# Performance work log

Measured on AMD Instinct MI355X. Metric: run time of the kernel, lower is better.

## Reference

```python
import jax, jax.numpy as jnp
import numpy as np
import math

N, E, R = 50000, 800000, 32
DIN = 128
H, D = 8, 16          # num_heads, head_dim; H*D == out_ent_feats == 128
HOP = 5
ALPHA = 0.1
EPS = 1e-5


def layer_norm(x, g, b):
    m = jnp.mean(x, axis=-1, keepdims=True)
    v = jnp.mean((x - m) ** 2, axis=-1, keepdims=True)
    return (x - m) * jax.lax.rsqrt(v + EPS) * g + b


def segment_softmax(e, dst, num_nodes):
    # e: [E, H] scores, softmax over incoming edges of each dst node
    m = jax.ops.segment_max(e, dst, num_segments=num_nodes)      # [N, H]
    ex = jnp.exp(e - m[dst])
    s = jax.ops.segment_sum(ex, dst, num_segments=num_nodes)     # [N, H]
    return ex / s[dst]


def setup_inputs() -> dict:
    key = jax.random.key(0)
    ks = jax.random.split(key, 12)
    gain = 0.02  # small init scale (small_init_gain-style)
    ent_feat = jax.random.normal(ks[0], (N, DIN), dtype=jnp.float32)
    rel_feat = jax.random.normal(ks[1], (R, DIN), dtype=jnp.float32)
    src = jax.random.randint(ks[2], (E,), 0, N, dtype=jnp.int32)
    # guarantee every node has in-degree >= 1 (DGL raises otherwise)
    dst_rand = jax.random.randint(ks[3], (E - N,), 0, N, dtype=jnp.int32)
    dst = jnp.concatenate([jnp.arange(N, dtype=jnp.int32), dst_rand])
    rid = jax.random.randint(ks[4], (E,), 0, R, dtype=jnp.int32)
    W_head = jax.random.normal(ks[5], (DIN, H * D), dtype=jnp.float32) * gain
    W_tail = jax.random.normal(ks[6], (DIN, H * D), dtype=jnp.float32) * gain
    W_ent = jax.random.normal(ks[7], (DIN, H * D), dtype=jnp.float32) * gain
    W_rel = jax.random.normal(ks[8], (DIN, H * D), dtype=jnp.float32) * gain
    attn_r = jax.random.normal(ks[9], (1, H, D), dtype=jnp.float32) * gain
    W1 = jax.random.normal(ks[10], (H * D, 4 * H * D), dtype=jnp.float32) * gain
    W2 = jax.random.normal(ks[11], (4 * H * D, H * D), dtype=jnp.float32) * gain
    return dict(
        ent_feat=ent_feat, rel_feat=rel_feat, src=src, dst=dst, rid=rid,
        W_head=W_head, W_tail=W_tail, W_ent=W_ent, W_rel=W_rel, attn_r=attn_r,
        ln_ent_g=jnp.ones((DIN,), jnp.float32), ln_ent_b=jnp.zeros((DIN,), jnp.float32),
        ln_rel_g=jnp.ones((DIN,), jnp.float32), ln_rel_b=jnp.zeros((DIN,), jnp.float32),
        ff_ln_g=jnp.ones((H * D,), jnp.float32), ff_ln_b=jnp.zeros((H * D,), jnp.float32),
        W1=W1, b1=jnp.zeros((4 * H * D,), jnp.float32),
        W2=W2, b2=jnp.zeros((H * D,), jnp.float32),
    )


def _forward(ent_feat, rel_feat, src, dst, rid,
             W_head, W_tail, W_ent, W_rel, attn_r,
             ln_ent_g, ln_ent_b, ln_rel_g, ln_rel_b, ff_ln_g, ff_ln_b,
             W1, b1, W2, b2):
    n = ent_feat.shape[0]
    x = layer_norm(ent_feat, ln_ent_g, ln_ent_b)
    feat_head = (x @ W_head).reshape(n, H, D)
    feat_tail = (x @ W_tail).reshape(n, H, D)
    feat_ent = (x @ W_ent).reshape(n, H, D)

    # per-edge dot-product attention score: u_dot_v('eh','et')
    e = jnp.sum(feat_head[src] * feat_tail[dst], axis=-1)          # [E, H]

    r = layer_norm(rel_feat, ln_rel_g, ln_rel_b)
    feat_rel = (r @ W_rel).reshape(R, H, D)
    er = jnp.sum(feat_rel * attn_r, axis=-1)                       # [R, H]
    e = e * er[rid]                                                # [E, H]

    # e_mul_v with log_in = log(in_degree) of dst node
    deg = jax.ops.segment_sum(jnp.ones((e.shape[0],), e.dtype), dst, num_segments=n)
    log_in = jnp.log(jnp.maximum(deg, 1.0))                        # [N]
    e = e * log_in[dst][:, None] / math.sqrt(D)

    a = segment_softmax(e, dst, n)                                 # [E, H]

    # PPR diffusion: feat <- (1-alpha) * A^T feat + alpha * feat_0
    feat = feat_ent
    for _ in range(HOP):
        msg = feat[src] * a[:, :, None]                            # [E, H, D]
        agg = jax.ops.segment_sum(msg, dst, num_segments=n)        # [N, H, D]
        feat = (1.0 - ALPHA) * agg + ALPHA * feat_ent

    # residual (Identity: in_ent_feats == out_ent_feats)
    rst = feat + ent_feat.reshape(n, H, D)
    rst = rst.reshape(n, H * D)

    h = layer_norm(rst, ff_ln_g, ff_ln_b)
    ff = jax.nn.relu(h @ W1 + b1) @ W2 + b2
    return ff + rst


def reference(ent_feat, rel_feat, src, dst, rid,
              W_head, W_tail, W_ent, W_rel, attn_r,
              ln_ent_g, ln_ent_b, ln_rel_g, ln_rel_b, ff_ln_g, ff_ln_b,
              W1, b1, W2, b2):
    return _forward(ent_feat, rel_feat, src, dst, rid,
                    W_head, W_tail, W_ent, W_rel, attn_r,
                    ln_ent_g, ln_ent_b, ln_rel_g, ln_rel_b, ff_ln_g, ff_ln_b,
                    W1, b1, W2, b2)
```

## Files before the change

kernel.cpp:

```cpp
#include <hip/hip_runtime.h>
#include <hip/hip_bf16.h>

#define N_NODES 50000
#define N_EDGES 800000
#define N_REL 32
#define DIN 128
#define NH 8
#define HD 16
#define FF_HID 512
#define EPS_LN 1e-5f

typedef __attribute__((ext_vector_type(8))) short bf16x8;
typedef __attribute__((ext_vector_type(4))) float f32x4;
typedef __attribute__((ext_vector_type(2))) float f32x2;
typedef unsigned short ushort_t;
typedef unsigned int uint_t;

static __device__ __forceinline__ unsigned short f2bf(float f) {
    union { float f; unsigned u; } v; v.f = f;
    unsigned r = (v.u + 0x7fffu + ((v.u >> 16) & 1u)) >> 16;
    return (unsigned short)r;
}
static __device__ __forceinline__ float bf2f(unsigned u16) {
    union { unsigned u; float f; } v; v.u = u16 << 16; return v.f;
}
static __device__ __forceinline__ unsigned char f2fp8(float f) {
    return (unsigned char)(__builtin_amdgcn_cvt_pk_fp8_f32(f, f, 0, false) & 0xff);
}
static __device__ __forceinline__ ushort_t f2fp8x2(float x0, float x1) {
    return (ushort_t)(__builtin_amdgcn_cvt_pk_fp8_f32(x0, x1, 0, false) & 0xffff);
}

static __device__ __forceinline__ void pack_dev(const float* __restrict__ W,
                                                short* __restrict__ out, int K, int Ncols,
                                                int idx) {
    int KT = K >> 5;
    int l = idx & 63;
    int tile = idx >> 6;
    int kt = tile & (KT - 1);
    int ct = tile / KT;
    int c = ct * 16 + (l & 15);
    int k0 = kt * 32 + ((l >> 4) * 8);
    bf16x8 v;
#pragma unroll
    for (int j = 0; j < 8; j++) v[j] = (short)f2bf(W[(size_t)(k0 + j) * Ncols + c]);
    *(bf16x8*)(out + (size_t)idx * 8) = v;
}

#define C0_HIST 512
__global__ __launch_bounds__(256) void combo0_kernel(
    const int* __restrict__ dst, int* __restrict__ deg, const float* __restrict__ W1,
    short* __restrict__ W1p, const float* __restrict__ W2, short* __restrict__ W2p,
    const float* __restrict__ Wh, short* __restrict__ Whp, const float* __restrict__ Wt,
    short* __restrict__ Wtp, const float* __restrict__ We, short* __restrict__ Wep,
    const float* __restrict__ rel_feat, const float* __restrict__ gr,
    const float* __restrict__ br, const float* __restrict__ W_rel,
    const float* __restrict__ attn_r, float* __restrict__ er) {
    __shared__ float red[128];
    __shared__ float xsr[128];
    __shared__ float prod[128];
    int b = blockIdx.x, tid = threadIdx.x;
    if (b < C0_HIST) {
        int i = b * 256 + tid;
        int stride = C0_HIST * 256;
        for (; i < N_EDGES; i += stride) atomicAdd(&deg[dst[i]], 1);
    } else if (b < C0_HIST + 32) {
        pack_dev(W1, W1p, DIN, FF_HID, (b - C0_HIST) * 256 + tid);
    } else if (b < C0_HIST + 64) {
        pack_dev(W2, W2p, FF_HID, DIN, (b - C0_HIST - 32) * 256 + tid);
    } else if (b < C0_HIST + 72) {
        pack_dev(Wh, Whp, DIN, DIN, (b - C0_HIST - 64) * 256 + tid);
    } else if (b < C0_HIST + 80) {
        pack_dev(Wt, Wtp, DIN, DIN, (b - C0_HIST - 72) * 256 + tid);
    } else if (b < C0_HIST + 88) {
        pack_dev(We, Wep, DIN, DIN, (b - C0_HIST - 80) * 256 + tid);
    } else {
        int r = b - (C0_HIST + 88);
        float x = 0.f;
        if (tid < 128) {
            x = rel_feat[r * DIN + tid];
            red[tid] = x;
        }
        __syncthreads();
        for (int off = 64; off > 0; off >>= 1) {
            if (tid < off) red[tid] += red[tid + off];
            __syncthreads();
        }
        float mean = red[0] * (1.f / DIN);
        __syncthreads();
        if (tid < 128) red[tid] = x * x;
        __syncthreads();
        for (int off = 64; off > 0; off >>= 1) {
            if (tid < off) red[tid] += red[tid + off];
            __syncthreads();
        }
        float var = red[0] * (1.f / DIN) - mean * mean;
        float rs = rsqrtf(var + EPS_LN);
        if (tid < 128) xsr[tid] = (x - mean) * rs * gr[tid] + br[tid];
        __syncthreads();
        if (tid < 128) {
            float acc = 0.f;
            for (int k = 0; k < DIN; k++) acc += xsr[k] * W_rel[k * DIN + tid];
            prod[tid] = acc * attn_r[tid];
        }
        __syncthreads();
        if (tid < NH) {
            float s = 0.f;
            for (int d = 0; d < HD; d++) s += prod[tid * HD + d];
            er[r * NH + tid] = s;
        }
    }
}

__global__ __launch_bounds__(1024) void scan2_kernel(const int* __restrict__ deg,
                                                     int* __restrict__ row_off, int n) {
    __shared__ int lds[1024];
    __shared__ int wsum[16];
    __shared__ int s_base;
    int b = blockIdx.x, tid = threadIdx.x;
    int start = b * 1024;
    int partial = 0;
    for (int i = tid; i < start; i += 1024) partial += deg[i];
    for (int m = 32; m > 0; m >>= 1) partial += __shfl_down(partial, m);
    int wid = tid >> 6, lane = tid & 63;
    if (lane == 0) wsum[wid] = partial;
    __syncthreads();
    if (tid == 0) {
        int s = 0;
#pragma unroll
        for (int w = 0; w < 16; w++) s += wsum[w];
        s_base = s;
    }
    int i = start + tid;
    int v = (i < n) ? deg[i] : 0;
    lds[tid] = v;
    __syncthreads();
    for (int off = 1; off < 1024; off <<= 1) {
        int t = (tid >= off) ? lds[tid - off] : 0;
        __syncthreads();
        lds[tid] += t;
        __syncthreads();
    }
    int base = s_base;
    if (i < n) row_off[i] = base + lds[tid] - v;
    if (i == n - 1) row_off[n] = base + lds[tid];
}

#define C1_SCAT 8192
#define NRANGE_DIV 6250
__global__ __launch_bounds__(256) void combo1_kernel(
    const int* __restrict__ src, const int* __restrict__ dst, const int* __restrict__ rid,
    const int* __restrict__ row_off, int* __restrict__ cursor, int* __restrict__ sr_perm,
    const float* __restrict__ ent, const float* __restrict__ g, const float* __restrict__ b,
    const short* __restrict__ Whp, const short* __restrict__ Wtp,
    const short* __restrict__ Wep, unsigned char* __restrict__ head_fp8,
    ushort_t* __restrict__ tail_bf, ushort_t* __restrict__ entp_bf,
    unsigned char* __restrict__ entp_fp8) {
    __shared__ float xs[32][128];
    __shared__ short hsb[32][136];
    int blk = blockIdx.x, tid = threadIdx.x;
    if (blk < C1_SCAT) {
        const int chunk = (N_EDGES + 1023) / 1024;
        int range = blk & 7;
        int slice = blk >> 3;
        int lo = range * NRANGE_DIV, hi = lo + NRANGE_DIV;
        int i0 = slice * chunk;
        int i1 = min(i0 + chunk, N_EDGES);
        for (int i = i0 + tid; i < i1; i += 256) {
            int u = dst[i];
            if (u >= lo && u < hi) {
                int p = row_off[u] + atomicAdd(&cursor[u], 1);
                sr_perm[p] = src[i] | (rid[i] << 16);
            }
        }
        return;
    }
    int base = (blk - C1_SCAT) * 32;
    {
        int c = tid & 127, rb = tid >> 7;
#pragma unroll
        for (int j = 0; j < 16; j++) {
            int r = j * 2 + rb;
            int row = base + r;
            xs[r][c] = (row < N_NODES) ? ent[(size_t)row * DIN + c] : 0.f;
        }
    }
    __syncthreads();
    int wave = tid >> 6, lane = tid & 63;
    {
        float g0 = g[lane], g1 = g[lane + 64], bb0 = b[lane], bb1 = b[lane + 64];
        for (int r = wave * 8; r < wave * 8 + 8; r++) {
            float x0 = xs[r][lane], x1 = xs[r][lane + 64];
            float s1 = x0 + x1, s2 = x0 * x0 + x1 * x1;
            for (int m = 1; m < 64; m <<= 1) {
                s1 += __shfl_xor(s1, m);
                s2 += __shfl_xor(s2, m);
            }
            float mean = s1 * (1.f / DIN);
            float var = s2 * (1.f / DIN) - mean * mean;
            float rs = rsqrtf(var + EPS_LN);
            hsb[r][lane] = (short)f2bf((x0 - mean) * rs * g0 + bb0);
            hsb[r][lane + 64] = (short)f2bf((x1 - mean) * rs * g1 + bb1);
        }
    }
    __syncthreads();
    bf16x8 a[2][4];
#pragma unroll
    for (int rt = 0; rt < 2; rt++)
#pragma unroll
        for (int kt = 0; kt < 4; kt++)
            a[rt][kt] = *(const bf16x8*)&hsb[rt * 16 + (lane & 15)][kt * 32 + (lane >> 4) * 8];
#pragma unroll
    for (int m = 0; m < 3; m++) {
        const bf16x8* bp = (m == 0)   ? (const bf16x8*)Whp
                           : (m == 1) ? (const bf16x8*)Wtp
                                      : (const bf16x8*)Wep;
#pragma unroll
        for (int c2 = 0; c2 < 2; c2++) {
            int ct = wave * 2 + c2;
            f32x4 acc0 = {0.f, 0.f, 0.f, 0.f}, acc1 = {0.f, 0.f, 0.f, 0.f};
#pragma unroll
            for (int kt = 0; kt < 4; kt++) {
                bf16x8 bf = bp[(ct * 4 + kt) * 64 + lane];
                acc0 = __builtin_amdgcn_mfma_f32_16x16x32_bf16(a[0][kt], bf, acc0, 0, 0, 0);
                acc1 = __builtin_amdgcn_mfma_f32_16x16x32_bf16(a[1][kt], bf, acc1, 0, 0, 0);
            }
            int col = ct * 16 + (lane & 15);
            int r0 = (lane >> 4) * 4;
#pragma unroll
            for (int j = 0; j < 4; j++) {
                int row0 = base + r0 + j, row1 = base + 16 + r0 + j;
                if (m == 0) {
                    if (row0 < N_NODES) head_fp8[(size_t)row0 * DIN + col] = f2fp8(acc0[j]);
                    if (row1 < N_NODES) head_fp8[(size_t)row1 * DIN + col] = f2fp8(acc1[j]);
                } else if (m == 1) {
                    if (row0 < N_NODES) tail_bf[(size_t)row0 * DIN + col] = f2bf(acc0[j]);
                    if (row1 < N_NODES) tail_bf[(size_t)row1 * DIN + col] = f2bf(acc1[j]);
                } else {
                    if (row0 < N_NODES) {
                        entp_bf[(size_t)row0 * DIN + col] = f2bf(acc0[j]);
                        entp_fp8[(size_t)row0 * DIN + col] = f2fp8(acc0[j]);
                    }
                    if (row1 < N_NODES) {
                        entp_bf[(size_t)row1 * DIN + col] = f2bf(acc1[j]);
                        entp_fp8[(size_t)row1 * DIN + col] = f2fp8(acc1[j]);
                    }
                }
            }
        }
    }
}

__global__ __launch_bounds__(256) void scores_kernel(
    const unsigned char* __restrict__ head_fp8, const ushort_t* __restrict__ tail_bf,
    const float* __restrict__ er, const int* __restrict__ row_off,
    const int* __restrict__ sr_perm, ushort_t* __restrict__ a_bf,
    float* __restrict__ inv9) {
    int wid = threadIdx.x >> 6;
    int u = blockIdx.x * 4 + wid;
    int lane = threadIdx.x & 63;
    int h = lane & 7, esub = lane >> 3;
    int p0 = row_off[u], p1 = row_off[u + 1];
    int deg = p1 - p0;
    float scale = logf((float)(deg > 0 ? deg : 1)) * 0.25f;
    float t[16];
    {
        const uint_t* tp = (const uint_t*)(tail_bf + (size_t)u * DIN + h * HD);
#pragma unroll
        for (int i = 0; i < 8; i++) {
            uint_t w = tp[i];
            t[2 * i] = bf2f(w & 0xffffu);
            t[2 * i + 1] = bf2f(w >> 16);
        }
    }
    float ssum = 0.f;
    for (int p = p0 + esub; p < p1; p += 8) {
        int v = sr_perm[p];
        int s = v & 0xffff;
        int rr = v >> 16;
        const uint_t* hp = (const uint_t*)(head_fp8 + (size_t)s * DIN + h * HD);
        float dot = 0.f;
#pragma unroll
        for (int i = 0; i < 4; i++) {
            uint_t w = hp[i];
            f32x2 lo = __builtin_amdgcn_cvt_pk_f32_fp8(w, false);
            f32x2 hi = __builtin_amdgcn_cvt_pk_f32_fp8(w, true);
            dot += lo.x * t[4 * i] + lo.y * t[4 * i + 1] + hi.x * t[4 * i + 2] +
                   hi.y * t[4 * i + 3];
        }
        float e = dot * er[rr * NH + h] * scale;
        float sx = expf(e);
        a_bf[(size_t)p * NH + h] = f2bf(sx);
        ssum += sx;
    }
    ssum += __shfl_xor(ssum, 8);
    ssum += __shfl_xor(ssum, 16);
    ssum += __shfl_xor(ssum, 32);
    if (lane < 8) inv9[(size_t)u * NH + lane] = 0.9f / ssum;
}

template <bool OUT_BF>
__global__ __launch_bounds__(256) void diffuse8_kernel(
    const unsigned char* __restrict__ fin8, const ushort_t* __restrict__ entp_bf,
    const ushort_t* __restrict__ a_bf, const int* __restrict__ sr_perm,
    const int* __restrict__ row_off, const float* __restrict__ inv9,
    void* __restrict__ fout) {
    int wid = threadIdx.x >> 6;
    int u = blockIdx.x * 4 + wid;
    int lane = threadIdx.x & 63;
    int hh = lane >> 3;
    int p0 = row_off[u], p1 = row_off[u + 1];
    float acc0 = 0.f, acc1 = 0.f;
    int p = p0;
    for (; p + 8 <= p1; p += 8) {
        int sv[8];
        float av[8];
        ushort_t wv[8];
#pragma unroll
        for (int k = 0; k < 8; k++) sv[k] = sr_perm[p + k] & 0xffff;
#pragma unroll
        for (int k = 0; k < 8; k++) av[k] = bf2f(a_bf[(size_t)(p + k) * NH + hh]);
#pragma unroll
        for (int k = 0; k < 8; k++)
            wv[k] = *(const ushort_t*)(fin8 + (size_t)sv[k] * DIN + 2 * lane);
#pragma unroll
        for (int k = 0; k < 8; k++) {
            f32x2 v = __builtin_amdgcn_cvt_pk_f32_fp8(wv[k], false);
            acc0 += av[k] * v.x;
            acc1 += av[k] * v.y;
        }
    }
    for (; p < p1; ++p) {
        int s0 = sr_perm[p] & 0xffff;
        float a0 = bf2f(a_bf[(size_t)p * NH + hh]);
        uint_t w0 = *(const ushort_t*)(fin8 + (size_t)s0 * DIN + 2 * lane);
        f32x2 v0 = __builtin_amdgcn_cvt_pk_f32_fp8(w0, false);
        acc0 += a0 * v0.x;
        acc1 += a0 * v0.y;
    }
    float iv = inv9[(size_t)u * NH + hh];
    size_t o = (size_t)u * DIN + 2 * lane;
    uint_t e = *(const uint_t*)(entp_bf + o);
    float x0 = iv * acc0 + 0.1f * bf2f(e & 0xffffu);
    float x1 = iv * acc1 + 0.1f * bf2f(e >> 16);
    if (OUT_BF) {
        *(uint_t*)((ushort_t*)fout + o) = (uint_t)f2bf(x0) | ((uint_t)f2bf(x1) << 16);
    } else {
        *(ushort_t*)((unsigned char*)fout + o) = f2fp8x2(x0, x1);
    }
}

static __device__ __forceinline__ int hid_idx(int row, int col) {
    return row * 512 + ((((col >> 3) & 63) ^ (row & 7)) << 3) + (col & 7);
}
__global__ __launch_bounds__(256) void ffn_mfma_kernel(
    const ushort_t* __restrict__ feat, const float* __restrict__ ent0,
    const float* __restrict__ g, const float* __restrict__ b,
    const short* __restrict__ W1p, const float* __restrict__ b1,
    const short* __restrict__ W2p, const float* __restrict__ b2,
    float* __restrict__ out) {
    __shared__ ushort_t rst_bf[16][136];
    __shared__ short hs[16][136];
    __shared__ short hid[16 * 512];
    int tid = threadIdx.x;
    int base = blockIdx.x * 16;
    int wave = tid >> 6, lane = tid & 63;
    {
        int c = tid & 127, rb = tid >> 7;
#pragma unroll
        for (int j = 0; j < 8; j++) {
            int r = j * 2 + rb;
            int row = base + r;
            float v = 0.f;
            if (row < N_NODES) {
                size_t idx = (size_t)row * DIN + c;
                v = bf2f(feat[idx]) + ent0[idx];
            }
            rst_bf[r][c] = f2bf(v);
        }
    }
    __syncthreads();
    {
        float g0 = g[lane], g1 = g[lane + 64], bb0 = b[lane], bb1 = b[lane + 64];
        for (int r = wave * 4; r < wave * 4 + 4; r++) {
            float x0 = bf2f(rst_bf[r][lane]), x1 = bf2f(rst_bf[r][lane + 64]);
            float s1 = x0 + x1, s2 = x0 * x0 + x1 * x1;
            for (int m = 1; m < 64; m <<= 1) {
                s1 += __shfl_xor(s1, m);
                s2 += __shfl_xor(s2, m);
            }
            float mean = s1 * (1.f / DIN);
            float var = s2 * (1.f / DIN) - mean * mean;
            float rs = rsqrtf(var + EPS_LN);
            hs[r][lane] = (short)f2bf((x0 - mean) * rs * g0 + bb0);
            hs[r][lane + 64] = (short)f2bf((x1 - mean) * rs * g1 + bb1);
        }
    }
    __syncthreads();
    {
        bf16x8 a[4];
#pragma unroll
        for (int kt = 0; kt < 4; kt++)
            a[kt] = *(const bf16x8*)&hs[lane & 15][kt * 32 + (lane >> 4) * 8];
        const bf16x8* bp = (const bf16x8*)W1p;
        for (int cti = 0; cti < 8; cti++) {
            int ct = wave * 8 + cti;
            f32x4 acc0 = {0.f, 0.f, 0.f, 0.f};
#pragma unroll
            for (int kt = 0; kt < 4; kt++) {
                bf16x8 bf = bp[(ct * 4 + kt) * 64 + lane];
                acc0 = __builtin_amdgcn_mfma_f32_16x16x32_bf16(a[kt], bf, acc0, 0, 0, 0);
            }
            int col = ct * 16 + (lane & 15);
            float bv = b1[col];
            int r0 = (lane >> 4) * 4;
#pragma unroll
            for (int j = 0; j < 4; j++)
                hid[hid_idx(r0 + j, col)] = (short)f2bf(fmaxf(acc0[j] + bv, 0.f));
        }
    }
    __syncthreads();
    {
        f32x4 acc[2] = {{0.f, 0.f, 0.f, 0.f}, {0.f, 0.f, 0.f, 0.f}};
        const bf16x8* bp2 = (const bf16x8*)W2p;
        for (int kt = 0; kt < 16; kt++) {
            int col8 = kt * 32 + (lane >> 4) * 8;
            bf16x8 a0 = *(const bf16x8*)&hid[hid_idx(lane & 15, col8)];
#pragma unroll
            for (int c2 = 0; c2 < 2; c2++) {
                int ct = wave * 2 + c2;
                bf16x8 bf = bp2[(ct * 16 + kt) * 64 + lane];
                acc[c2] = __builtin_amdgcn_mfma_f32_16x16x32_bf16(a0, bf, acc[c2], 0, 0, 0);
            }
        }
#pragma unroll
        for (int c2 = 0; c2 < 2; c2++) {
            int col = (wave * 2 + c2) * 16 + (lane & 15);
            float bv = b2[col];
            int r0 = (lane >> 4) * 4;
#pragma unroll
            for (int j = 0; j < 4; j++) {
                int row = base + r0 + j;
                if (row < N_NODES)
                    out[(size_t)row * DIN + col] = acc[c2][j] + bv + bf2f(rst_bf[r0 + j][col]);
            }
        }
    }
}

extern "C" void kernel_launch(void* const* d_in, const int* in_sizes, int n_in,
                              void* d_out, int out_size, void* d_ws, size_t ws_size,
                              hipStream_t stream) {
    const float* ent_feat = (const float*)d_in[0];
    const float* rel_feat = (const float*)d_in[1];
    const int* src = (const int*)d_in[2];
    const int* dst = (const int*)d_in[3];
    const int* rid = (const int*)d_in[4];
    const float* W_head = (const float*)d_in[5];
    const float* W_tail = (const float*)d_in[6];
    const float* W_ent = (const float*)d_in[7];
    const float* W_rel = (const float*)d_in[8];
    const float* attn_r = (const float*)d_in[9];
    const float* ln_ent_g = (const float*)d_in[10];
    const float* ln_ent_b = (const float*)d_in[11];
    const float* ln_rel_g = (const float*)d_in[12];
    const float* ln_rel_b = (const float*)d_in[13];
    const float* ff_ln_g = (const float*)d_in[14];
    const float* ff_ln_b = (const float*)d_in[15];
    const float* W1 = (const float*)d_in[16];
    const float* b1 = (const float*)d_in[17];
    const float* W2 = (const float*)d_in[18];
    const float* b2 = (const float*)d_in[19];
    float* out = (float*)d_out;

    const int N = N_NODES, E = N_EDGES;

    char* cur = (char*)d_ws;
    auto alloc = [&](size_t bytes, size_t align) -> void* {
        uintptr_t p = (uintptr_t)cur;
        p = (p + align - 1) & ~(uintptr_t)(align - 1);
        cur = (char*)(p + bytes);
        return (void*)p;
    };
    ushort_t* tail_bf = (ushort_t*)alloc((size_t)N * DIN * 2, 16);
    ushort_t* entp_bf = (ushort_t*)alloc((size_t)N * DIN * 2, 16);
    unsigned char* entp_fp8 = (unsigned char*)alloc((size_t)N * DIN, 16);
    unsigned char* f8A = (unsigned char*)alloc((size_t)N * DIN, 16);
    unsigned char* f8B = (unsigned char*)alloc((size_t)N * DIN, 16);
    unsigned char* head_fp8 = (unsigned char*)alloc((size_t)N * DIN, 16);
    int* sr_perm = (int*)alloc((size_t)E * 4, 16);
    int* row_off = (int*)alloc((size_t)(N + 1) * 4, 16);
    int* deg = (int*)alloc((size_t)2 * N * 4, 16);
    int* cursor = deg + N;
    float* er = (float*)alloc((size_t)N_REL * NH * 4, 16);
    float* inv9 = (float*)alloc((size_t)N * NH * 4, 16);
    short* W1p = (short*)alloc((size_t)DIN * FF_HID * 2, 16);
    short* W2p = (short*)alloc((size_t)FF_HID * DIN * 2, 16);
    short* Whp = (short*)alloc((size_t)DIN * DIN * 2, 16);
    short* Wtp = (short*)alloc((size_t)DIN * DIN * 2, 16);
    short* Wep = (short*)alloc((size_t)DIN * DIN * 2, 16);
    ushort_t* a_fit = (ushort_t*)alloc((size_t)E * NH * 2, 16);
    ushort_t* a_bf = ((size_t)(cur - (char*)d_ws) <= ws_size) ? a_fit : (ushort_t*)d_out;

    hipMemsetAsync(deg, 0, sizeof(int) * 2 * (size_t)N, stream);
    combo0_kernel<<<632, 256, 0, stream>>>(dst, deg, W1, W1p, W2, W2p, W_head, Whp,
                                           W_tail, Wtp, W_ent, Wep, rel_feat, ln_rel_g,
                                           ln_rel_b, W_rel, attn_r, er);
    scan2_kernel<<<(N + 1023) / 1024, 1024, 0, stream>>>(deg, row_off, N);
    int nblk32 = (N + 31) / 32;
    combo1_kernel<<<C1_SCAT + nblk32, 256, 0, stream>>>(
        src, dst, rid, row_off, cursor, sr_perm, ent_feat, ln_ent_g, ln_ent_b, Whp, Wtp,
        Wep, head_fp8, tail_bf, entp_bf, entp_fp8);
    scores_kernel<<<N / 4, 256, 0, stream>>>(head_fp8, tail_bf, er, row_off, sr_perm,
                                             a_bf, inv9);
    diffuse8_kernel<false><<<N / 4, 256, 0, stream>>>(entp_fp8, entp_bf, a_bf, sr_perm,
                                                      row_off, inv9, f8A);
    diffuse8_kernel<false><<<N / 4, 256, 0, stream>>>(f8A, entp_bf, a_bf, sr_perm,
                                                      row_off, inv9, f8B);
    diffuse8_kernel<false><<<N / 4, 256, 0, stream>>>(f8B, entp_bf, a_bf, sr_perm,
                                                      row_off, inv9, f8A);
    diffuse8_kernel<false><<<N / 4, 256, 0, stream>>>(f8A, entp_bf, a_bf, sr_perm,
                                                      row_off, inv9, f8B);
    diffuse8_kernel<true><<<N / 4, 256, 0, stream>>>(f8B, entp_bf, a_bf, sr_perm,
                                                     row_off, inv9, tail_bf);
    int nblk16 = (N + 15) / 16;
    ffn_mfma_kernel<<<nblk16, 256, 0, stream>>>(tail_bf, ent_feat, ff_ln_g, ff_ln_b, W1p,
                                                b1, W2p, b2, out);
}
```

Before: 365.5 us.

## Bucket edges by destination range during histogram; widen diffusion gathers to 8 bytes

The histogram pass now also bins each edge (dst, packed src/rid) into one of eight destination-range buckets, using LDS counters and one global atomic per bucket per round. The CSR scatter then reads only its own bucket instead of rescanning every edge eight times with range filters. The diffusion kernel now has four lane groups each handle a different edge, with every lane loading 8 fp8 features, followed by a cross-group shuffle reduction. This cuts redundant edge reads and raises bytes per gather, at the cost of an extra bucket buffer of fixed capacity that could overflow on skewed inputs and more syncthreads in the binning loop.

```diff
diff --git a/kernel.cpp b/kernel.cpp
--- a/kernel.cpp
+++ b/kernel.cpp
@@ -9,6 +9,9 @@
 #define HD 16
 #define FF_HID 512
 #define EPS_LN 1e-5f
+#define NBUCK 8
+#define BDIV 6250
+#define BCAP 114688
 
 typedef __attribute__((ext_vector_type(8))) short bf16x8;
 typedef __attribute__((ext_vector_type(4))) float f32x4;
@@ -27,8 +30,8 @@
 static __device__ __forceinline__ unsigned char f2fp8(float f) {
     return (unsigned char)(__builtin_amdgcn_cvt_pk_fp8_f32(f, f, 0, false) & 0xff);
 }
-static __device__ __forceinline__ ushort_t f2fp8x2(float x0, float x1) {
-    return (ushort_t)(__builtin_amdgcn_cvt_pk_fp8_f32(x0, x1, 0, false) & 0xffff);
+static __device__ __forceinline__ uint_t f2fp8x2(float x0, float x1) {
+    return (__builtin_amdgcn_cvt_pk_fp8_f32(x0, x1, 0, false) & 0xffffu);
 }
 
 static __device__ __forceinline__ void pack_dev(const float* __restrict__ W,
@@ -47,35 +50,59 @@
     *(bf16x8*)(out + (size_t)idx * 8) = v;
 }
 
-#define C0_HIST 512
+#define C0_BIN 512
 __global__ __launch_bounds__(256) void combo0_kernel(
-    const int* __restrict__ dst, int* __restrict__ deg, const float* __restrict__ W1,
-    short* __restrict__ W1p, const float* __restrict__ W2, short* __restrict__ W2p,
-    const float* __restrict__ Wh, short* __restrict__ Whp, const float* __restrict__ Wt,
-    short* __restrict__ Wtp, const float* __restrict__ We, short* __restrict__ Wep,
-    const float* __restrict__ rel_feat, const float* __restrict__ gr,
-    const float* __restrict__ br, const float* __restrict__ W_rel,
-    const float* __restrict__ attn_r, float* __restrict__ er) {
+    const int* __restrict__ src, const int* __restrict__ dst, const int* __restrict__ rid,
+    int* __restrict__ deg, int* __restrict__ gcnt, int2* __restrict__ buck,
+    const float* __restrict__ W1, short* __restrict__ W1p, const float* __restrict__ W2,
+    short* __restrict__ W2p, const float* __restrict__ Wh, short* __restrict__ Whp,
+    const float* __restrict__ Wt, short* __restrict__ Wtp, const float* __restrict__ We,
+    short* __restrict__ Wep, const float* __restrict__ rel_feat,
+    const float* __restrict__ gr, const float* __restrict__ br,
+    const float* __restrict__ W_rel, const float* __restrict__ attn_r,
+    float* __restrict__ er) {
     __shared__ float red[128];
     __shared__ float xsr[128];
     __shared__ float prod[128];
+    __shared__ int cnt[NBUCK];
+    __shared__ int sbase[NBUCK];
     int b = blockIdx.x, tid = threadIdx.x;
-    if (b < C0_HIST) {
-        int i = b * 256 + tid;
-        int stride = C0_HIST * 256;
-        for (; i < N_EDGES; i += stride) atomicAdd(&deg[dst[i]], 1);
-    } else if (b < C0_HIST + 32) {
-        pack_dev(W1, W1p, DIN, FF_HID, (b - C0_HIST) * 256 + tid);
-    } else if (b < C0_HIST + 64) {
-        pack_dev(W2, W2p, FF_HID, DIN, (b - C0_HIST - 32) * 256 + tid);
-    } else if (b < C0_HIST + 72) {
-        pack_dev(Wh, Whp, DIN, DIN, (b - C0_HIST - 64) * 256 + tid);
-    } else if (b < C0_HIST + 80) {
-        pack_dev(Wt, Wtp, DIN, DIN, (b - C0_HIST - 72) * 256 + tid);
-    } else if (b < C0_HIST + 88) {
-        pack_dev(We, Wep, DIN, DIN, (b - C0_HIST - 80) * 256 + tid);
+    if (b < C0_BIN) {
+        const int chunk = (N_EDGES + C0_BIN - 1) / C0_BIN;
+        int i0 = b * chunk;
+        int i1 = min(i0 + chunk, N_EDGES);
+        int rounds = (i1 - i0 + 255) >> 8;
+        for (int r = 0; r < rounds; r++) {
+            int i = i0 + (r << 8) + tid;
+            if (tid < NBUCK) cnt[tid] = 0;
+            __syncthreads();
+            int d = 0, b8 = 0, rank = 0, py = 0;
+            bool v = i < i1;
+            if (v) {
+                d = dst[i];
+                b8 = d / BDIV;
+                py = src[i] | (rid[i] << 16);
+                rank = atomicAdd(&cnt[b8], 1);
+                atomicAdd(&deg[d], 1);
+            }
+            __syncthreads();
+            if (tid < NBUCK) sbase[tid] = atomicAdd(&gcnt[tid], cnt[tid]);
+            __syncthreads();
+            if (v) buck[(size_t)b8 * BCAP + sbase[b8] + rank] = make_int2(d, py);
+            __syncthreads();
+        }
+    } else if (b < C0_BIN + 32) {
+        pack_dev(W1, W1p, DIN, FF_HID, (b - C0_BIN) * 256 + tid);
+    } else if (b < C0_BIN + 64) {
+        pack_dev(W2, W2p, FF_HID, DIN, (b - C0_BIN - 32) * 256 + tid);
+    } else if (b < C0_BIN + 72) {
+        pack_dev(Wh, Whp, DIN, DIN, (b - C0_BIN - 64) * 256 + tid);
+    } else if (b < C0_BIN + 80) {
+        pack_dev(Wt, Wtp, DIN, DIN, (b - C0_BIN - 72) * 256 + tid);
+    } else if (b < C0_BIN + 88) {
+        pack_dev(We, Wep, DIN, DIN, (b - C0_BIN - 80) * 256 + tid);
     } else {
-        int r = b - (C0_HIST + 88);
+        int r = b - (C0_BIN + 88);
         float x = 0.f;
         if (tid < 128) {
             x = rel_feat[r * DIN + tid];
@@ -146,10 +173,9 @@
     if (i == n - 1) row_off[n] = base + lds[tid];
 }
 
-#define C1_SCAT 8192
-#define NRANGE_DIV 6250
+#define C1_SCAT 1024
 __global__ __launch_bounds__(256) void combo1_kernel(
-    const int* __restrict__ src, const int* __restrict__ dst, const int* __restrict__ rid,
+    const int2* __restrict__ buck, const int* __restrict__ gcnt,
     const int* __restrict__ row_off, int* __restrict__ cursor, int* __restrict__ sr_perm,
     const float* __restrict__ ent, const float* __restrict__ g, const float* __restrict__ b,
     const short* __restrict__ Whp, const short* __restrict__ Wtp,
@@ -160,18 +186,16 @@
     __shared__ short hsb[32][136];
     int blk = blockIdx.x, tid = threadIdx.x;
     if (blk < C1_SCAT) {
-        const int chunk = (N_EDGES + 1023) / 1024;
-        int range = blk & 7;
-        int slice = blk >> 3;
-        int lo = range * NRANGE_DIV, hi = lo + NRANGE_DIV;
-        int i0 = slice * chunk;
-        int i1 = min(i0 + chunk, N_EDGES);
+        int b8 = blk & 7, sub = blk >> 3;
+        int cnt = gcnt[b8];
+        int chunk = (cnt + 127) >> 7;
+        int i0 = sub * chunk;
+        int i1 = min(i0 + chunk, cnt);
+        const int2* bp = buck + (size_t)b8 * BCAP;
         for (int i = i0 + tid; i < i1; i += 256) {
-            int u = dst[i];
-            if (u >= lo && u < hi) {
-                int p = row_off[u] + atomicAdd(&cursor[u], 1);
-                sr_perm[p] = src[i] | (rid[i] << 16);
-            }
+            int2 e = bp[i];
+            int p = row_off[e.x] + atomicAdd(&cursor[e.x], 1);
+            sr_perm[p] = e.y;
         }
         return;
     }
@@ -300,7 +324,7 @@
 }
 
 template <bool OUT_BF>
-__global__ __launch_bounds__(256) void diffuse8_kernel(
+__global__ __launch_bounds__(256) void diffuse4_kernel(
     const unsigned char* __restrict__ fin8, const ushort_t* __restrict__ entp_bf,
     const ushort_t* __restrict__ a_bf, const int* __restrict__ sr_perm,
     const int* __restrict__ row_off, const float* __restrict__ inv9,
@@ -308,45 +332,57 @@
     int wid = threadIdx.x >> 6;
     int u = blockIdx.x * 4 + wid;
     int lane = threadIdx.x & 63;
-    int hh = lane >> 3;
+    int c = lane & 15;
+    int g = lane >> 4;
+    int hh = c >> 1;
     int p0 = row_off[u], p1 = row_off[u + 1];
-    float acc0 = 0.f, acc1 = 0.f;
-    int p = p0;
-    for (; p + 8 <= p1; p += 8) {
-        int sv[8];
-        float av[8];
-        ushort_t wv[8];
-#pragma unroll
-        for (int k = 0; k < 8; k++) sv[k] = sr_perm[p + k] & 0xffff;
-#pragma unroll
-        for (int k = 0; k < 8; k++) av[k] = bf2f(a_bf[(size_t)(p + k) * NH + hh]);
-#pragma unroll
-        for (int k = 0; k < 8; k++)
-            wv[k] = *(const ushort_t*)(fin8 + (size_t)sv[k] * DIN + 2 * lane);
-#pragma unroll
-        for (int k = 0; k < 8; k++) {
-            f32x2 v = __builtin_amdgcn_cvt_pk_f32_fp8(wv[k], false);
-            acc0 += av[k] * v.x;
-            acc1 += av[k] * v.y;
-        }
-    }
-    for (; p < p1; ++p) {
-        int s0 = sr_perm[p] & 0xffff;
-        float a0 = bf2f(a_bf[(size_t)p * NH + hh]);
-        uint_t w0 = *(const ushort_t*)(fin8 + (size_t)s0 * DIN + 2 * lane);
-        f32x2 v0 = __builtin_amdgcn_cvt_pk_f32_fp8(w0, false);
-        acc0 += a0 * v0.x;
-        acc1 += a0 * v0.y;
-    }
-    float iv = inv9[(size_t)u * NH + hh];
-    size_t o = (size_t)u * DIN + 2 * lane;
-    uint_t e = *(const uint_t*)(entp_bf + o);
-    float x0 = iv * acc0 + 0.1f * bf2f(e & 0xffffu);
-    float x1 = iv * acc1 + 0.1f * bf2f(e >> 16);
-    if (OUT_BF) {
-        *(uint_t*)((ushort_t*)fout + o) = (uint_t)f2bf(x0) | ((uint_t)f2bf(x1) << 16);
-    } else {
-        *(ushort_t*)((unsigned char*)fout + o) = f2fp8x2(x0, x1);
+    float acc[8];
+#pragma unroll
+    for (int j = 0; j < 8; j++) acc[j] = 0.f;
+    for (int p = p0; p < p1; p += 4) {
+        int pe = p + g;
+        bool valid = pe < p1;
+        int pc = valid ? pe : (p1 - 1);
+        int s = sr_perm[pc] & 0xffff;
+        float a = valid ? bf2f(a_bf[(size_t)pc * NH + hh]) : 0.f;
+        uint2 w = *(const uint2*)(fin8 + (size_t)s * DIN + 8 * c);
+        f32x2 l0 = __builtin_amdgcn_cvt_pk_f32_fp8(w.x, false);
+        f32x2 h0 = __builtin_amdgcn_cvt_pk_f32_fp8(w.x, true);
+        f32x2 l1 = __builtin_amdgcn_cvt_pk_f32_fp8(w.y, false);
+        f32x2 h1 = __builtin_amdgcn_cvt_pk_f32_fp8(w.y, true);
+        acc[0] += a * l0.x; acc[1] += a * l0.y; acc[2] += a * h0.x; acc[3] += a * h0.y;
+        acc[4] += a * l1.x; acc[5] += a * l1.y; acc[6] += a * h1.x; acc[7] += a * h1.y;
+    }
+#pragma unroll
+    for (int j = 0; j < 8; j++) {
+        acc[j] += __shfl_xor(acc[j], 16);
+        acc[j] += __shfl_xor(acc[j], 32);
+    }
+    if (g == 0) {
+        float iv = inv9[(size_t)u * NH + hh];
+        size_t o = (size_t)u * DIN + 8 * c;
+        uint4 e4 = *(const uint4*)(entp_bf + o);
+        float x0 = iv * acc[0] + 0.1f * bf2f(e4.x & 0xffffu);
+        float x1 = iv * acc[1] + 0.1f * bf2f(e4.x >> 16);
+        float x2 = iv * acc[2] + 0.1f * bf2f(e4.y & 0xffffu);
+        float x3 = iv * acc[3] + 0.1f * bf2f(e4.y >> 16);
+        float x4 = iv * acc[4] + 0.1f * bf2f(e4.z & 0xffffu);
+        float x5 = iv * acc[5] + 0.1f * bf2f(e4.z >> 16);
+        float x6 = iv * acc[6] + 0.1f * bf2f(e4.w & 0xffffu);
+        float x7 = iv * acc[7] + 0.1f * bf2f(e4.w >> 16);
+        if (OUT_BF) {
+            uint4 ov;
+            ov.x = (uint_t)f2bf(x0) | ((uint_t)f2bf(x1) << 16);
+            ov.y = (uint_t)f2bf(x2) | ((uint_t)f2bf(x3) << 16);
+            ov.z = (uint_t)f2bf(x4) | ((uint_t)f2bf(x5) << 16);
+            ov.w = (uint_t)f2bf(x6) | ((uint_t)f2bf(x7) << 16);
+            *(uint4*)((ushort_t*)fout + o) = ov;
+        } else {
+            uint2 ov;
+            ov.x = f2fp8x2(x0, x1) | (f2fp8x2(x2, x3) << 16);
+            ov.y = f2fp8x2(x4, x5) | (f2fp8x2(x6, x7) << 16);
+            *(uint2*)((unsigned char*)fout + o) = ov;
+        }
     }
 }
 
@@ -488,10 +524,12 @@
     unsigned char* f8A = (unsigned char*)alloc((size_t)N * DIN, 16);
     unsigned char* f8B = (unsigned char*)alloc((size_t)N * DIN, 16);
     unsigned char* head_fp8 = (unsigned char*)alloc((size_t)N * DIN, 16);
+    int2* buck = (int2*)alloc((size_t)NBUCK * BCAP * 8, 16);
     int* sr_perm = (int*)alloc((size_t)E * 4, 16);
     int* row_off = (int*)alloc((size_t)(N + 1) * 4, 16);
-    int* deg = (int*)alloc((size_t)2 * N * 4, 16);
+    int* deg = (int*)alloc(((size_t)2 * N + NBUCK) * 4, 16);
     int* cursor = deg + N;
+    int* gcnt = deg + 2 * N;
     float* er = (float*)alloc((size_t)N_REL * NH * 4, 16);
     float* inv9 = (float*)alloc((size_t)N * NH * 4, 16);
     short* W1p = (short*)alloc((size_t)DIN * FF_HID * 2, 16);
@@ -502,26 +540,27 @@
     ushort_t* a_fit = (ushort_t*)alloc((size_t)E * NH * 2, 16);
     ushort_t* a_bf = ((size_t)(cur - (char*)d_ws) <= ws_size) ? a_fit : (ushort_t*)d_out;
 
-    hipMemsetAsync(deg, 0, sizeof(int) * 2 * (size_t)N, stream);
-    combo0_kernel<<<632, 256, 0, stream>>>(dst, deg, W1, W1p, W2, W2p, W_head, Whp,
-                                           W_tail, Wtp, W_ent, Wep, rel_feat, ln_rel_g,
-                                           ln_rel_b, W_rel, attn_r, er);
+    hipMemsetAsync(deg, 0, sizeof(int) * ((size_t)2 * N + NBUCK), stream);
+    combo0_kernel<<<632, 256, 0, stream>>>(src, dst, rid, deg, gcnt, buck, W1, W1p, W2,
+                                           W2p, W_head, Whp, W_tail, Wtp, W_ent, Wep,
+                                           rel_feat, ln_rel_g, ln_rel_b, W_rel, attn_r,
+                                           er);
     scan2_kernel<<<(N + 1023) / 1024, 1024, 0, stream>>>(deg, row_off, N);
     int nblk32 = (N + 31) / 32;
     combo1_kernel<<<C1_SCAT + nblk32, 256, 0, stream>>>(
-        src, dst, rid, row_off, cursor, sr_perm, ent_feat, ln_ent_g, ln_ent_b, Whp, Wtp,
+        buck, gcnt, row_off, cursor, sr_perm, ent_feat, ln_ent_g, ln_ent_b, Whp, Wtp,
         Wep, head_fp8, tail_bf, entp_bf, entp_fp8);
     scores_kernel<<<N / 4, 256, 0, stream>>>(head_fp8, tail_bf, er, row_off, sr_perm,
                                              a_bf, inv9);
-    diffuse8_kernel<false><<<N / 4, 256, 0, stream>>>(entp_fp8, entp_bf, a_bf, sr_perm,
+    diffuse4_kernel<false><<<N / 4, 256, 0, stream>>>(entp_fp8, entp_bf, a_bf, sr_perm,
                                                       row_off, inv9, f8A);
-    diffuse8_kernel<false><<<N / 4, 256, 0, stream>>>(f8A, entp_bf, a_bf, sr_perm,
+    diffuse4_kernel<false><<<N / 4, 256, 0, stream>>>(f8A, entp_bf, a_bf, sr_perm,
                                                       row_off, inv9, f8B);
-    diffuse8_kernel<false><<<N / 4, 256, 0, stream>>>(f8B, entp_bf, a_bf, sr_perm,
+    diffuse4_kernel<false><<<N / 4, 256, 0, stream>>>(f8B, entp_bf, a_bf, sr_perm,
                                                       row_off, inv9, f8A);
-    diffuse8_kernel<false><<<N / 4, 256, 0, stream>>>(f8A, entp_bf, a_bf, sr_perm,
+    diffuse4_kernel<false><<<N / 4, 256, 0, stream>>>(f8A, entp_bf, a_bf, sr_perm,
                                                       row_off, inv9, f8B);
-    diffuse8_kernel<true><<<N / 4, 256, 0, stream>>>(f8B, entp_bf, a_bf, sr_perm,
+    diffuse4_kernel<true><<<N / 4, 256, 0, stream>>>(f8B, entp_bf, a_bf, sr_perm,
                                                      row_off, inv9, tail_bf);
     int nblk16 = (N + 15) / 16;
     ffn_mfma_kernel<<<nblk16, 256, 0, stream>>>(tail_bf, ent_feat, ff_ln_g, ff_ln_b, W1p,
```

After: 369.2 us. No clear change (+1.0%).
